# Kernel tuning notes

Hardware: AMD Instinct MI355X
Metric: run time of the kernel (lower is better)

Reference implementation:

```python
import jax, jax.numpy as jnp
import numpy as np

IMAGE_SIZE = 800
OUT = 50          # feature map size
FEAT = 512
SCALES = (2.0, 4.0, 6.0)
RATIOS = (0.5, 1.0, 1.5)
A = len(SCALES) * len(RATIOS)          # 9 anchors per cell
POS_THR, NEG_THR = 0.7, 0.3
W_CONF, W_REG = 1.0, 5.0
SCALE = IMAGE_SIZE // OUT              # 16, stride of feature map


def _anchor_base():
    # order: ratio outer loop, scale inner loop (matches get_anchor_base)
    ws = jnp.array([s * r for r in RATIOS for s in SCALES], jnp.float32)  # [A]
    hs = jnp.array([s for r in RATIOS for s in SCALES], jnp.float32)      # [A]
    cx = (jnp.arange(OUT, dtype=jnp.float32) + 0.5)[:, None, None]        # grid dim0 -> x
    cy = (jnp.arange(OUT, dtype=jnp.float32) + 0.5)[None, :, None]        # grid dim1 -> y
    xmin = jnp.clip(cx - ws / 2, 0.0, OUT)
    xmax = jnp.clip(cx + ws / 2, 0.0, OUT)
    ymin = jnp.clip(cy - hs / 2, 0.0, OUT)
    ymax = jnp.clip(cy + hs / 2, 0.0, OUT)
    shp = (OUT, OUT, A)
    base = jnp.stack([jnp.broadcast_to(xmin, shp), jnp.broadcast_to(ymin, shp),
                      jnp.broadcast_to(xmax, shp), jnp.broadcast_to(ymax, shp)], axis=-1)
    return base.reshape(-1, 4)         # [N,4], N = OUT*OUT*A = 22500


def _iou(anchors, gt):
    # anchors [N,4], gt [B,M,4] (xyxy) -> iou [B,N,M]
    a = anchors[None, :, None, :]
    g = gt[:, None, :, :]
    ix1 = jnp.maximum(a[..., 0], g[..., 0]); iy1 = jnp.maximum(a[..., 1], g[..., 1])
    ix2 = jnp.minimum(a[..., 2], g[..., 2]); iy2 = jnp.minimum(a[..., 3], g[..., 3])
    inter = jnp.clip(ix2 - ix1, 0.0) * jnp.clip(iy2 - iy1, 0.0)
    area_a = (a[..., 2] - a[..., 0]) * (a[..., 3] - a[..., 1])
    area_g = (g[..., 2] - g[..., 0]) * (g[..., 3] - g[..., 1])
    return inter / (area_a + area_g - inter + 1e-8)


def _smooth_l1(d):
    ad = jnp.abs(d)
    return jnp.where(ad < 1.0, 0.5 * d * d, ad - 0.5)


def setup_inputs() -> dict:
    key = jax.random.key(0)
    ks = jax.random.split(key, 8)
    B, M = 16, 16
    features = jax.random.normal(ks[0], (B, FEAT, OUT, OUT), jnp.float32)
    # valid GT boxes in image coords: centers in [100,700], sizes in [32,200]
    cxy = jax.random.uniform(ks[1], (B, M, 2), jnp.float32, 100.0, 700.0)
    wh = jax.random.uniform(ks[2], (B, M, 2), jnp.float32, 32.0, 200.0)
    x1y1 = jnp.clip(cxy - wh / 2, 0.0, IMAGE_SIZE)
    x2y2 = jnp.clip(cxy + wh / 2, 0.0, IMAGE_SIZE)
    gt_boxes = jnp.concatenate([x1y1, x2y2], axis=-1)
    w1 = jax.random.normal(ks[3], (FEAT, FEAT, 3, 3), jnp.float32) * 0.02
    b1 = jnp.zeros((FEAT,), jnp.float32)
    w_cls = jax.random.normal(ks[4], (A, FEAT), jnp.float32) * 0.02
    b_cls = jnp.zeros((A,), jnp.float32)
    w_box = jax.random.normal(ks[5], (4 * A, FEAT), jnp.float32) * 0.02
    b_box = jnp.zeros((4 * A,), jnp.float32)
    return {"features": features, "gt_boxes": gt_boxes, "w1": w1, "b1": b1,
            "w_cls": w_cls, "b_cls": b_cls, "w_box": w_box, "b_box": b_box}


def reference(features, gt_boxes, w1, b1, w_cls, b_cls, w_box, b_box):
    B = features.shape[0]
    anchors = _anchor_base()                                   # [N,4]
    N = anchors.shape[0]

    # --- conv tower ---
    x = jax.lax.conv_general_dilated(features, w1, (1, 1), 'SAME') + b1[None, :, None, None]
    cls_map = jnp.einsum('bchw,ac->bahw', x, w_cls) + b_cls[None, :, None, None]   # [B,A,H,W]
    box_map = jnp.einsum('bchw,dc->bdhw', x, w_box) + b_box[None, :, None, None]   # [B,4A,H,W]
    logits = jnp.transpose(cls_map, (0, 2, 3, 1)).reshape(B, N)                    # [B,N]
    pred_off = jnp.transpose(box_map.reshape(B, A, 4, OUT, OUT), (0, 3, 4, 1, 2)).reshape(B, N, 4)

    # --- project gt to feature-map (anchor) coords, 'p2a' ---
    gt = gt_boxes / SCALE                                       # [B,M,4]

    # --- anchor/GT assignment ---
    iou = _iou(anchors, gt)                                     # [B,N,M]
    max_per_gt = jnp.max(iou, axis=1, keepdims=True)            # best anchor per gt
    pos_mask = ((iou == max_per_gt) & (max_per_gt > 0)) | (iou > POS_THR)  # [B,N,M]
    pos_mask = pos_mask.astype(jnp.float32)
    n_pos = jnp.maximum(pos_mask.sum(), 1.0)

    # --- gt offsets (standard tx,ty,tw,th) for every (anchor,gt) pair ---
    acx = (anchors[:, 0] + anchors[:, 2]) / 2
    acy = (anchors[:, 1] + anchors[:, 3]) / 2
    aw = jnp.maximum(anchors[:, 2] - anchors[:, 0], 1e-6)
    ah = jnp.maximum(anchors[:, 3] - anchors[:, 1], 1e-6)
    gcx = (gt[..., 0] + gt[..., 2]) / 2                         # [B,M]
    gcy = (gt[..., 1] + gt[..., 3]) / 2
    gw = jnp.maximum(gt[..., 2] - gt[..., 0], 1e-6)
    gh = jnp.maximum(gt[..., 3] - gt[..., 1], 1e-6)
    tx = (gcx[:, None, :] - acx[None, :, None]) / aw[None, :, None]   # [B,N,M]
    ty = (gcy[:, None, :] - acy[None, :, None]) / ah[None, :, None]
    tw = jnp.log(gw[:, None, :] / aw[None, :, None])
    th = jnp.log(gh[:, None, :] / ah[None, :, None])
    gt_off = jnp.stack([tx, ty, tw, th], axis=-1)               # [B,N,M,4]

    diff = gt_off - pred_off[:, :, None, :]
    reg_loss = (pos_mask[..., None] * _smooth_l1(diff)).sum() / (4.0 * n_pos)

    # --- classification loss: BCE-with-logits; positives=1, negatives=0 ---
    pos_loss = (pos_mask * jax.nn.softplus(-logits)[:, :, None]).sum() / n_pos
    neg_anchor = jnp.all(iou < NEG_THR, axis=2).astype(jnp.float32)   # [B,N]
    n_neg = jnp.maximum(neg_anchor.sum(), 1.0)
    neg_loss = (neg_anchor * jax.nn.softplus(logits)).sum() / n_neg
    cls_loss = 0.5 * (pos_loss + neg_loss)

    total_rpn_loss = W_CONF * cls_loss + W_REG * reg_loss

    # --- proposals from predicted offsets for all anchors ---
    pcx = acx[None, :] + pred_off[..., 0] * aw[None, :]
    pcy = acy[None, :] + pred_off[..., 1] * ah[None, :]
    pw = aw[None, :] * jnp.exp(pred_off[..., 2])
    ph = ah[None, :] * jnp.exp(pred_off[..., 3])
    proposals = jnp.stack([pcx - pw / 2, pcy - ph / 2, pcx + pw / 2, pcy + ph / 2], axis=-1)  # [B,N,4]

    return total_rpn_loss, proposals
```

## Files before the change

kernel.cpp:

```cpp
#include <hip/hip_runtime.h>
#include <hip/hip_bf16.h>
#include <stdint.h>


using bf16x8 = __attribute__((ext_vector_type(8))) __bf16;
using f32x4  = __attribute__((ext_vector_type(4))) float;

#define FT_CHUNK_STRIDE 2768896
#define W2_CHUNK_B 27648

__device__ __forceinline__ unsigned short f2bf(float f) {
  union { float f; unsigned u; } x; x.f = f;
  unsigned r = x.u + 0x7fffu + ((x.u >> 16) & 1u);
  return (unsigned short)(r >> 16);
}

__device__ __forceinline__ void gl_lds16(const void* g, void* l) {
  __builtin_amdgcn_global_load_lds(
      (const __attribute__((address_space(1))) void*)g,
      (__attribute__((address_space(3))) void*)l, 16, 0, 0);
}

__device__ __forceinline__ float sl1(float d) {
  float ad = fabsf(d);
  return ad < 1.f ? 0.5f * d * d : ad - 0.5f;
}
__device__ __forceinline__ float softplus_f(float x) {
  return fmaxf(x, 0.f) + log1pf(expf(-fabsf(x)));
}

__device__ __forceinline__ void anchor_strict(int n, float& ax1, float& ay1,
                                              float& ax2, float& ay2) {
  int ii = n / 450;
  int rem = n - ii * 450;
  int jj = rem / 9;
  int a  = rem - jj * 9;
  const float SC[3] = {2.f, 4.f, 6.f};
  const float RA[3] = {0.5f, 1.f, 1.5f};
  float w = __fmul_rn(SC[a % 3], RA[a / 3]);
  float h = SC[a % 3];
  float cx = __fadd_rn((float)ii, 0.5f);
  float cy = __fadd_rn((float)jj, 0.5f);
  float wh = __fmul_rn(w, 0.5f), hh = __fmul_rn(h, 0.5f);
  ax1 = fminf(fmaxf(__fsub_rn(cx, wh), 0.f), 50.f);
  ax2 = fminf(fmaxf(__fadd_rn(cx, wh), 0.f), 50.f);
  ay1 = fminf(fmaxf(__fsub_rn(cy, hh), 0.f), 50.f);
  ay2 = fminf(fmaxf(__fadd_rn(cy, hh), 0.f), 50.f);
}
__device__ __forceinline__ float iou_pre(float ax1, float ay1, float ax2, float ay2,
                                         float aarea, const float* __restrict__ s) {
  float ix1 = fmaxf(ax1, s[0]), iy1 = fmaxf(ay1, s[1]);
  float ix2 = fminf(ax2, s[2]), iy2 = fminf(ay2, s[3]);
  float inter = __fmul_rn(fmaxf(__fsub_rn(ix2, ix1), 0.f),
                          fmaxf(__fsub_rn(iy2, iy1), 0.f));
  float denom = __fadd_rn(__fsub_rn(__fadd_rn(aarea, s[4]), inter), 1e-8f);
  return __fdiv_rn(inter, denom);
}

__global__ __launch_bounds__(256, 6) void k1a(const float* __restrict__ feat,
                                              char* __restrict__ featT2) {
  __shared__ __align__(16) unsigned short sT[64 * 132];
  const int bx = blockIdx.x;
  const int tid = threadIdx.x;
  const int tile = bx % 41;
  const int rest = bx / 41;
  const int g    = rest & 3;
  const int b    = rest >> 2;
  if (tile == 40) {
    uint4 z = {0, 0, 0, 0};
    for (int u = tid; u < 204 * 4; u += 256) {
      int p = u & 255; if (p >= 204) p -= 204;
      int c4 = u / 204;
      int ip, jp;
      if (p < 52)       { ip = 0;       jp = p; }
      else if (p < 104) { ip = 51;      jp = p - 52; }
      else if (p < 154) { ip = p - 103; jp = 0; }
      else              { ip = p - 153; jp = 51; }
      char* dst = featT2 + (size_t)(g * 4 + c4) * FT_CHUNK_STRIDE
                + (size_t)(b * 2704 + ip * 52 + jp) * 64;
      *(uint4*)(dst)      = z;
      *(uint4*)(dst + 16) = z;
      *(uint4*)(dst + 32) = z;
      *(uint4*)(dst + 48) = z;
    }
    return;
  }
  const int pos0 = tile * 64;
  const float* fb = feat + (size_t)b * 1280000 + (size_t)(g * 128) * 2500;
  const int pq = tid & 15;
  const int cq = tid >> 4;
  const int p  = pos0 + pq * 4;
  float vv[2][4][4];
  if (p + 3 < 2500) {
#pragma unroll
    for (int it = 0; it < 2; ++it)
#pragma unroll
      for (int q = 0; q < 4; ++q) {
        float4 v = *(const float4*)(fb + (size_t)(it * 64 + cq * 4 + q) * 2500 + p);
        vv[it][q][0] = v.x; vv[it][q][1] = v.y;
        vv[it][q][2] = v.z; vv[it][q][3] = v.w;
      }
  } else {
#pragma unroll
    for (int it = 0; it < 2; ++it)
#pragma unroll
      for (int q = 0; q < 4; ++q)
#pragma unroll
        for (int e = 0; e < 4; ++e)
          vv[it][q][e] = fb[(size_t)(it * 64 + cq * 4 + q) * 2500 + min(p + e, 2499)];
  }
#pragma unroll
  for (int it = 0; it < 2; ++it) {
#pragma unroll
    for (int pp = 0; pp < 4; ++pp) {
      ushort4 pk;
      pk.x = f2bf(vv[it][0][pp]); pk.y = f2bf(vv[it][1][pp]);
      pk.z = f2bf(vv[it][2][pp]); pk.w = f2bf(vv[it][3][pp]);
      *(ushort4*)&sT[(pq * 4 + pp) * 132 + it * 64 + cq * 4] = pk;
    }
  }
  __syncthreads();
  {
    int ch = tid >> 6, pr = tid & 63;
    int gp = pos0 + pr;
    if (gp < 2500) {
      int i = gp / 50, j = gp - i * 50;
      char* dst = featT2 + (size_t)(g * 4 + ch) * FT_CHUNK_STRIDE
                + (size_t)(b * 2704 + (i + 1) * 52 + (j + 1)) * 64;
      const uint4* src = (const uint4*)&sT[pr * 132 + ch * 32];
      uint4 a0 = src[0], a1 = src[1], a2 = src[2], a3 = src[3];
      *(uint4*)(dst)      = a0;
      *(uint4*)(dst + 16) = a1;
      *(uint4*)(dst + 32) = a2;
      *(uint4*)(dst + 48) = a3;
    }
  }
}

__global__ __launch_bounds__(256, 4) void k1b(const float* __restrict__ w1,
                                              const float* __restrict__ wc,
                                              const float* __restrict__ wb,
                                              const float* __restrict__ b1,
                                              const float* __restrict__ bc,
                                              const float* __restrict__ bbx,
                                              float* __restrict__ part,
                                              float* __restrict__ bias_eff,
                                              const float* __restrict__ gt_boxes,
                                              float* __restrict__ iouBuf,
                                              float* __restrict__ mxPart,
                                              unsigned* __restrict__ accz) {
  __shared__ __align__(16) float sW[48 * 64];
  const int bxr = blockIdx.x;
  const int tid = threadIdx.x;

  if (bxr < 576) {
    if (bxr == 0 && tid < 8) accz[tid] = 0u;
    int cz = bxr / 72, kx = bxr - cz * 72;
#pragma unroll
    for (int q = 0; q < 12; ++q) {
      int idx = tid + q * 256;
      int co = idx >> 6, cl = idx & 63;
      int c = cz * 64 + cl;
      float v = 0.f;
      if (co < 9) v = wc[co * 512 + c];
      else if (co < 45) v = wb[(co - 9) * 512 + c];
      sW[co * 64 + cl] = v;
    }
    __syncthreads();
    const int kmem = kx * 64 + (tid & 63);
    const int coq  = tid >> 6;
    float acc[12];
#pragma unroll
    for (int j = 0; j < 12; ++j) acc[j] = 0.f;
    const float* w1p = w1 + (size_t)(cz * 64) * 4608 + kmem;
    for (int c4 = 0; c4 < 64; c4 += 4) {
      float f0 = w1p[(size_t)(c4 + 0) * 4608];
      float f1 = w1p[(size_t)(c4 + 1) * 4608];
      float f2 = w1p[(size_t)(c4 + 2) * 4608];
      float f3 = w1p[(size_t)(c4 + 3) * 4608];
#pragma unroll
      for (int j = 0; j < 12; ++j) {
        float4 wv = *(const float4*)&sW[(coq * 12 + j) * 64 + c4];
        acc[j] += wv.x * f0 + wv.y * f1 + wv.z * f2 + wv.w * f3;
      }
    }
    float* dst = part + (size_t)cz * 221184 + kmem;
#pragma unroll
    for (int j = 0; j < 12; ++j) dst[(size_t)(coq * 12 + j) * 4608] = acc[j];
    return;
  }

  if (bxr < 624) {
    int co = bxr - 576;
    int l = tid;
    if (l >= 64) return;
    float s = 0.f;
#pragma unroll
    for (int q = 0; q < 8; ++q) {
      int c = q * 64 + l;
      float wv = co < 9 ? wc[co * 512 + c] : (co < 45 ? wb[(co - 9) * 512 + c] : 0.f);
      s += wv * b1[c];
    }
    for (int o = 32; o; o >>= 1) s += __shfl_down(s, o, 64);
    if (l == 0)
      bias_eff[co] = s + (co < 9 ? bc[co] : (co < 45 ? bbx[co - 9] : 0.f));
    return;
  }

  {
    int q = bxr - 624;
    int b = q / 88, nb = q - b * 88;
    int n = nb * 256 + tid;
    float (*sgg)[5] = (float(*)[5])sW;
    float (*red)[16] = (float(*)[16])(sW + 128);
    if (tid < 16) {
      const float* g = gt_boxes + (b * 16 + tid) * 4;
      float gx1 = __fmul_rn(g[0], 0.0625f), gy1 = __fmul_rn(g[1], 0.0625f);
      float gx2 = __fmul_rn(g[2], 0.0625f), gy2 = __fmul_rn(g[3], 0.0625f);
      sgg[tid][0] = gx1; sgg[tid][1] = gy1; sgg[tid][2] = gx2; sgg[tid][3] = gy2;
      sgg[tid][4] = __fmul_rn(__fsub_rn(gx2, gx1), __fsub_rn(gy2, gy1));
    }
    __syncthreads();
    float lm[16];
#pragma unroll
    for (int m = 0; m < 16; ++m) lm[m] = 0.f;
    if (n < 22500) {
      float ax1, ay1, ax2, ay2;
      anchor_strict(n, ax1, ay1, ax2, ay2);
      float aarea = __fmul_rn(__fsub_rn(ax2, ax1), __fsub_rn(ay2, ay1));
#pragma unroll
      for (int m = 0; m < 16; ++m)
        lm[m] = iou_pre(ax1, ay1, ax2, ay2, aarea, sgg[m]);
      float* dv = iouBuf + (size_t)(b * 22500 + n) * 16;
#pragma unroll
      for (int v4 = 0; v4 < 4; ++v4) {
        float4 pk;
        pk.x = lm[v4 * 4 + 0]; pk.y = lm[v4 * 4 + 1];
        pk.z = lm[v4 * 4 + 2]; pk.w = lm[v4 * 4 + 3];
        *(float4*)(dv + v4 * 4) = pk;
      }
    }
#pragma unroll
    for (int m = 0; m < 16; ++m) {
      float v = lm[m];
      for (int o = 32; o; o >>= 1) v = fmaxf(v, __shfl_down(v, o, 64));
      if ((tid & 63) == 0) red[tid >> 6][m] = v;
    }
    __syncthreads();
    if (tid < 16) {
      float v = fmaxf(fmaxf(red[0][tid], red[1][tid]),
                      fmaxf(red[2][tid], red[3][tid]));
      mxPart[(b * 16 + tid) * 88 + nb] = v;
    }
  }
}

__global__ __launch_bounds__(256) void k2(const float* __restrict__ part,
                                          unsigned short* __restrict__ w2,
                                          const float* __restrict__ mxPart,
                                          unsigned* __restrict__ mx) {
  if (blockIdx.x == 864) {
    int t = threadIdx.x;
    const float* mp = mxPart + t * 88;
    float v = 0.f;
    for (int k = 0; k < 88; ++k) v = fmaxf(v, mp[k]);
    mx[t] = __float_as_uint(v);
    return;
  }
  int co = blockIdx.x / 18, kx = blockIdx.x - co * 18;
  int kmem = kx * 256 + threadIdx.x;
  const float* p = part + (size_t)co * 4608 + kmem;
  float s = 0.f;
#pragma unroll
  for (int cz = 0; cz < 8; ++cz) s += p[(size_t)cz * 221184];
  int ci = kmem / 9, tap = kmem - ci * 9;
  int c = ci >> 5, e = ci & 31;
  int boff = c * W2_CHUNK_B + tap * 3072 + (co >> 4) * 1024 + (co & 15) * 64
           + ((((e >> 3) ^ co) & 3) << 4) + ((e & 7) << 1);
  w2[boff >> 1] = f2bf(s);
}

__global__ __launch_bounds__(256, 2) void k3(const char* __restrict__ featT2,
                                             const char* __restrict__ w2g,
                                             const float* __restrict__ beff,
                                             float* __restrict__ oh) {
  __shared__ __align__(16) char sF[2][11264];
  __shared__ __align__(16) char sA[2][27648];
  const int tid = threadIdx.x, lane = tid & 63, w = tid >> 6;
  const int bx0 = blockIdx.x;
  const int bx = ((bx0 & 7) << 6) | (bx0 >> 3);
  const int b = bx >> 5, tl = bx & 31, tr = tl >> 3, tc = tl & 7;
  const int i0 = tr * 13 - (tr == 3 ? 1 : 0);
  const int TI = (tr >= 2) ? 12 : 13;
  const int TJ = (tc < 2) ? 7 : 6;
  const int j0 = (tc < 2) ? tc * 7 : 14 + (tc - 2) * 6;
  const int TJ2 = TJ + 2;
  const int mcount = TI * TJ;
  const int pieces = (TI + 2) * TJ2 * 5;

  const char* srcF[3];
#pragma unroll
  for (int k = 0; k < 3; ++k) {
    int s = w * 3 + k;
    int pi = s * 64 + lane;
    if (pi >= pieces) pi = pieces - 1;
    int pos = pi / 5, pc = pi - pos * 5;
    if (pc > 3) pc = 3;
    int hi = pos / TJ2, hj = pos - hi * TJ2;
    srcF[k] = featT2 + (size_t)(b * 2704 + (i0 + hi) * 52 + (j0 + hj)) * 64 + pc * 16;
  }
  int idxB[2];
#pragma unroll
  for (int bf = 0; bf < 2; ++bf) {
    int p = (w * 2 + bf) * 16 + (lane & 15);
    if (p >= mcount) p = mcount - 1;
    int di = p / TJ, dj = p - di * TJ;
    idxB[bf] = (di * TJ2 + dj) * 80 + (lane >> 4) * 16;
  }
  const int aoff = (lane & 15) * 64 + ((((lane >> 4) ^ lane) & 3) << 4);
  int toff[9];
#pragma unroll
  for (int tp = 0; tp < 9; ++tp) toff[tp] = ((tp / 3) * TJ2 + (tp % 3)) * 80;

  f32x4 acc[3][2] = {};

  auto stage = [&](int c, int pb) {
    size_t coff = (size_t)c * FT_CHUNK_STRIDE;
#pragma unroll
    for (int k = 0; k < 3; ++k) {
      int s = w * 3 + k;
      if (s < 11) gl_lds16(srcF[k] + coff, sF[pb] + s * 1024);
    }
#pragma unroll
    for (int k = 0; k < 7; ++k) {
      int s = w + 4 * k;
      if (s < 27)
        gl_lds16(w2g + (size_t)c * W2_CHUNK_B + s * 1024 + lane * 16, sA[pb] + s * 1024);
    }
  };

  stage(0, 0);
  __builtin_amdgcn_s_waitcnt(0);
  __syncthreads();

  for (int c = 0; c < 16; ++c) {
    int pb = c & 1;
    if (c < 15) stage(c + 1, pb ^ 1);
    const char* fA = sA[pb];
    const char* fB = sF[pb];
#pragma unroll
    for (int tp = 0; tp < 9; ++tp) {
      bf16x8 av[3], bv[2];
#pragma unroll
      for (int cf = 0; cf < 3; ++cf)
        av[cf] = *(const bf16x8*)(fA + tp * 3072 + cf * 1024 + aoff);
#pragma unroll
      for (int bf = 0; bf < 2; ++bf)
        bv[bf] = *(const bf16x8*)(fB + idxB[bf] + toff[tp]);
#pragma unroll
      for (int cf = 0; cf < 3; ++cf)
#pragma unroll
        for (int bf = 0; bf < 2; ++bf)
          acc[cf][bf] = __builtin_amdgcn_mfma_f32_16x16x32_bf16(av[cf], bv[bf], acc[cf][bf], 0, 0, 0);
    }
    __builtin_amdgcn_s_waitcnt(0);
    __syncthreads();
  }

  f32x4 bias[3];
#pragma unroll
  for (int cf = 0; cf < 3; ++cf)
    bias[cf] = *(const f32x4*)(beff + cf * 16 + (lane >> 4) * 4);
#pragma unroll
  for (int bf = 0; bf < 2; ++bf) {
    int p = (w * 2 + bf) * 16 + (lane & 15);
    if (p >= mcount) continue;
    int di = p / TJ, dj = p - di * TJ;
    int gm = (b * 50 + i0 + di) * 50 + (j0 + dj);
#pragma unroll
    for (int cf = 0; cf < 3; ++cf) {
      f32x4 v = acc[cf][bf];
#pragma unroll
      for (int r = 0; r < 4; ++r) v[r] += bias[cf][r];
      *(f32x4*)(oh + (size_t)gm * 48 + cf * 16 + (lane >> 4) * 4) = v;
    }
  }
}

__global__ __launch_bounds__(256, 2) void k4(const float* __restrict__ gt_boxes,
                                             const unsigned* __restrict__ mxbuf,
                                             const float* __restrict__ iouBuf,
                                             const float* __restrict__ oh,
                                             float* __restrict__ accum,
                                             float* __restrict__ dout) {
  const int tid = threadIdx.x;
  const int b = blockIdx.y;
  __shared__ float sg[16][5];
  if (tid < 16) {
    const float* g = gt_boxes + (b * 16 + tid) * 4;
    float gx1 = __fmul_rn(g[0], 0.0625f), gy1 = __fmul_rn(g[1], 0.0625f);
    float gx2 = __fmul_rn(g[2], 0.0625f), gy2 = __fmul_rn(g[3], 0.0625f);
    sg[tid][0] = (gx1 + gx2) * 0.5f;
    sg[tid][1] = (gy1 + gy2) * 0.5f;
    sg[tid][2] = fmaxf(gx2 - gx1, 1e-6f);
    sg[tid][3] = fmaxf(gy2 - gy1, 1e-6f);
    sg[tid][4] = __uint_as_float(mxbuf[b * 16 + tid]);
  }
  __syncthreads();

  const int n = blockIdx.x * 256 + tid;
  float s_np = 0.f, s_reg = 0.f, s_pos = 0.f, s_nc = 0.f, s_nl = 0.f;
  if (n < 22500) {
    float ax1, ay1, ax2, ay2;
    anchor_strict(n, ax1, ay1, ax2, ay2);
    float acx = (ax1 + ax2) * 0.5f, acy = (ay1 + ay2) * 0.5f;
    float aw = fmaxf(ax2 - ax1, 1e-6f), ah = fmaxf(ay2 - ay1, 1e-6f);
    int ii = n / 450, rem = n - ii * 450, jj = rem / 9, a = rem - jj * 9;
    const float* row = oh + ((size_t)(b * 2500 + ii * 50 + jj)) * 48;
    float logit = row[a];
    float p0 = row[9 + a * 4], p1 = row[10 + a * 4];
    float p2 = row[11 + a * 4], p3 = row[12 + a * 4];
    const float* iv = iouBuf + (size_t)(b * 22500 + n) * 16;
    float io[16];
#pragma unroll
    for (int v4 = 0; v4 < 4; ++v4) {
      float4 v = *(const float4*)(iv + v4 * 4);
      io[v4 * 4 + 0] = v.x; io[v4 * 4 + 1] = v.y;
      io[v4 * 4 + 2] = v.z; io[v4 * 4 + 3] = v.w;
    }
    int npos = 0;
    bool allneg = true;
#pragma unroll
    for (int m = 0; m < 16; ++m) {
      float iou = io[m];
      float mxv = sg[m][4];
      bool pos = ((iou == mxv) && (mxv > 0.f)) || (iou > 0.7f);
      if (iou >= 0.3f) allneg = false;
      if (pos) {
        ++npos;
        float tx = (sg[m][0] - acx) / aw, ty = (sg[m][1] - acy) / ah;
        float twv = logf(sg[m][2] / aw), thv = logf(sg[m][3] / ah);
        s_reg += sl1(tx - p0) + sl1(ty - p1) + sl1(twv - p2) + sl1(thv - p3);
      }
    }
    s_np = (float)npos;
    s_pos = (float)npos * softplus_f(-logit);
    if (allneg) { s_nc = 1.f; s_nl = softplus_f(logit); }
    float pcx = acx + p0 * aw, pcy = acy + p1 * ah;
    float pw = aw * expf(p2), ph = ah * expf(p3);
    float* o = dout + 1 + ((size_t)b * 22500 + n) * 4;
    o[0] = pcx - pw * 0.5f;
    o[1] = pcy - ph * 0.5f;
    o[2] = pcx + pw * 0.5f;
    o[3] = pcy + ph * 0.5f;
  }
  float vals[5] = {s_np, s_reg, s_pos, s_nc, s_nl};
  __shared__ float red[4][5];
#pragma unroll
  for (int q = 0; q < 5; ++q) {
    float v = vals[q];
    for (int o = 32; o; o >>= 1) v += __shfl_down(v, o, 64);
    if ((tid & 63) == 0) red[tid >> 6][q] = v;
  }
  __syncthreads();
  if (tid < 5) {
    float v = red[0][tid] + red[1][tid] + red[2][tid] + red[3][tid];
    atomicAdd(accum + tid, v);
  }
  __syncthreads();
  if (tid == 0) {
    __threadfence();
    unsigned old = atomicAdd((unsigned*)(accum + 5), 1u);
    if (old == 1407u) {
      float np = fmaxf(atomicAdd(accum + 0, 0.f), 1.f);
      float rg = atomicAdd(accum + 1, 0.f);
      float pp = atomicAdd(accum + 2, 0.f);
      float nn = fmaxf(atomicAdd(accum + 3, 0.f), 1.f);
      float nl = atomicAdd(accum + 4, 0.f);
      dout[0] = 0.5f * (pp / np + nl / nn) + 5.f * (rg / (4.f * np));
    }
  }
}

extern "C" void kernel_launch(void* const* d_in, const int* in_sizes, int n_in,
                              void* d_out, int out_size, void* d_ws, size_t ws_size,
                              hipStream_t stream) {
  const float* features = (const float*)d_in[0];
  const float* gt_boxes = (const float*)d_in[1];
  const float* w1    = (const float*)d_in[2];
  const float* b1    = (const float*)d_in[3];
  const float* w_cls = (const float*)d_in[4];
  const float* b_cls = (const float*)d_in[5];
  const float* w_box = (const float*)d_in[6];
  const float* b_box = (const float*)d_in[7];
  float* out = (float*)d_out;
  char* ws = (char*)d_ws;

  char*           featT2 = ws;
  unsigned short* w2     = (unsigned short*)(ws + 44302336);
  float*          wpart  = (float*)(ws + 44855296);
  float*          oh     = (float*)(ws + 51933184);
  float*          beff   = (float*)(ws + 59613184);
  float*          mxPart = (float*)(ws + 59613376);
  unsigned*       mx     = (unsigned*)(ws + 59703488);
  float*          accum  = (float*)(ws + 59704512);
  float*          iouBuf = (float*)(ws + 59704576);

  k1b<<<2032, 256, 0, stream>>>(w1, w_cls, w_box, b1, b_cls, b_box, wpart, beff,
                                gt_boxes, iouBuf, mxPart, (unsigned*)accum);
  k2<<<865, 256, 0, stream>>>(wpart, w2, mxPart, mx);
  k1a<<<2624, 256, 0, stream>>>(features, featT2);
  k3<<<512, 256, 0, stream>>>(featT2, (const char*)w2, beff, oh);
  k4<<<dim3(88, 16), 256, 0, stream>>>(gt_boxes, mx, iouBuf, oh, accum, out);
}
```

Baseline: 291.2 us.

## Merge preprocessing kernels into one launch and fold weight reduction inline

Combines the feature transpose, weight-folding, bias and IoU kernels into a single heterogeneous kernel with coarsened blocks (four work units per block). The weight fold now reduces all 512 channels per block and writes swizzled bf16 weights directly, which removes the partial-sum buffer and the separate reduction kernel. The per-GT max reduction moves into the loss kernel, which also processes four chunks per block with fewer atomics. This cuts launches and intermediate traffic, but the weight-fold path now runs on only 72 blocks with long serial loops, so it may become a critical-path straggler.

```diff
diff --git a/kernel.cpp b/kernel.cpp
--- a/kernel.cpp
+++ b/kernel.cpp
@@ -57,162 +57,185 @@
   return __fdiv_rn(inter, denom);
 }
 
-__global__ __launch_bounds__(256, 6) void k1a(const float* __restrict__ feat,
-                                              char* __restrict__ featT2) {
-  __shared__ __align__(16) unsigned short sT[64 * 132];
-  const int bx = blockIdx.x;
-  const int tid = threadIdx.x;
-  const int tile = bx % 41;
-  const int rest = bx / 41;
-  const int g    = rest & 3;
-  const int b    = rest >> 2;
-  if (tile == 40) {
-    uint4 z = {0, 0, 0, 0};
-    for (int u = tid; u < 204 * 4; u += 256) {
-      int p = u & 255; if (p >= 204) p -= 204;
-      int c4 = u / 204;
-      int ip, jp;
-      if (p < 52)       { ip = 0;       jp = p; }
-      else if (p < 104) { ip = 51;      jp = p - 52; }
-      else if (p < 154) { ip = p - 103; jp = 0; }
-      else              { ip = p - 153; jp = 51; }
-      char* dst = featT2 + (size_t)(g * 4 + c4) * FT_CHUNK_STRIDE
-                + (size_t)(b * 2704 + ip * 52 + jp) * 64;
-      *(uint4*)(dst)      = z;
-      *(uint4*)(dst + 16) = z;
-      *(uint4*)(dst + 32) = z;
-      *(uint4*)(dst + 48) = z;
-    }
-    return;
-  }
-  const int pos0 = tile * 64;
-  const float* fb = feat + (size_t)b * 1280000 + (size_t)(g * 128) * 2500;
-  const int pq = tid & 15;
-  const int cq = tid >> 4;
-  const int p  = pos0 + pq * 4;
-  float vv[2][4][4];
-  if (p + 3 < 2500) {
-#pragma unroll
-    for (int it = 0; it < 2; ++it)
-#pragma unroll
-      for (int q = 0; q < 4; ++q) {
-        float4 v = *(const float4*)(fb + (size_t)(it * 64 + cq * 4 + q) * 2500 + p);
-        vv[it][q][0] = v.x; vv[it][q][1] = v.y;
-        vv[it][q][2] = v.z; vv[it][q][3] = v.w;
-      }
-  } else {
-#pragma unroll
-    for (int it = 0; it < 2; ++it)
-#pragma unroll
-      for (int q = 0; q < 4; ++q)
-#pragma unroll
-        for (int e = 0; e < 4; ++e)
-          vv[it][q][e] = fb[(size_t)(it * 64 + cq * 4 + q) * 2500 + min(p + e, 2499)];
-  }
-#pragma unroll
-  for (int it = 0; it < 2; ++it) {
-#pragma unroll
-    for (int pp = 0; pp < 4; ++pp) {
-      ushort4 pk;
-      pk.x = f2bf(vv[it][0][pp]); pk.y = f2bf(vv[it][1][pp]);
-      pk.z = f2bf(vv[it][2][pp]); pk.w = f2bf(vv[it][3][pp]);
-      *(ushort4*)&sT[(pq * 4 + pp) * 132 + it * 64 + cq * 4] = pk;
-    }
-  }
-  __syncthreads();
-  {
-    int ch = tid >> 6, pr = tid & 63;
-    int gp = pos0 + pr;
-    if (gp < 2500) {
-      int i = gp / 50, j = gp - i * 50;
-      char* dst = featT2 + (size_t)(g * 4 + ch) * FT_CHUNK_STRIDE
-                + (size_t)(b * 2704 + (i + 1) * 52 + (j + 1)) * 64;
-      const uint4* src = (const uint4*)&sT[pr * 132 + ch * 32];
-      uint4 a0 = src[0], a1 = src[1], a2 = src[2], a3 = src[3];
-      *(uint4*)(dst)      = a0;
-      *(uint4*)(dst + 16) = a1;
-      *(uint4*)(dst + 32) = a2;
-      *(uint4*)(dst + 48) = a3;
-    }
-  }
-}
-
-__global__ __launch_bounds__(256, 4) void k1b(const float* __restrict__ w1,
-                                              const float* __restrict__ wc,
-                                              const float* __restrict__ wb,
-                                              const float* __restrict__ b1,
-                                              const float* __restrict__ bc,
-                                              const float* __restrict__ bbx,
-                                              float* __restrict__ part,
-                                              float* __restrict__ bias_eff,
-                                              const float* __restrict__ gt_boxes,
-                                              float* __restrict__ iouBuf,
-                                              float* __restrict__ mxPart,
-                                              unsigned* __restrict__ accz) {
-  __shared__ __align__(16) float sW[48 * 64];
+__global__ __launch_bounds__(256, 4) void kA(const float* __restrict__ feat,
+                                             char* __restrict__ featT2,
+                                             const float* __restrict__ w1,
+                                             const float* __restrict__ wc,
+                                             const float* __restrict__ wb,
+                                             const float* __restrict__ b1,
+                                             const float* __restrict__ bc,
+                                             const float* __restrict__ bbx,
+                                             unsigned short* __restrict__ w2,
+                                             float* __restrict__ bias_eff,
+                                             const float* __restrict__ gt_boxes,
+                                             float* __restrict__ iouBuf,
+                                             float* __restrict__ mxPart,
+                                             unsigned* __restrict__ accz) {
+  __shared__ __align__(16) char smem[24576];
   const int bxr = blockIdx.x;
   const int tid = threadIdx.x;
 
-  if (bxr < 576) {
-    if (bxr == 0 && tid < 8) accz[tid] = 0u;
-    int cz = bxr / 72, kx = bxr - cz * 72;
-#pragma unroll
-    for (int q = 0; q < 12; ++q) {
+  if (bxr < 656) {
+    unsigned short* sT = (unsigned short*)smem;
+#pragma unroll 1
+    for (int ku = 0; ku < 4; ++ku) {
+      if (ku) __syncthreads();
+      const int u = bxr * 4 + ku;
+      const int tile = u % 41;
+      const int rest = u / 41;
+      const int g    = rest & 3;
+      const int b    = rest >> 2;
+      if (tile == 40) {
+        uint4 z = {0, 0, 0, 0};
+        for (int uu = tid; uu < 204 * 4; uu += 256) {
+          int p = uu & 255; if (p >= 204) p -= 204;
+          int c4 = uu / 204;
+          int ip, jp;
+          if (p < 52)       { ip = 0;       jp = p; }
+          else if (p < 104) { ip = 51;      jp = p - 52; }
+          else if (p < 154) { ip = p - 103; jp = 0; }
+          else              { ip = p - 153; jp = 51; }
+          char* dst = featT2 + (size_t)(g * 4 + c4) * FT_CHUNK_STRIDE
+                    + (size_t)(b * 2704 + ip * 52 + jp) * 64;
+          *(uint4*)(dst)      = z;
+          *(uint4*)(dst + 16) = z;
+          *(uint4*)(dst + 32) = z;
+          *(uint4*)(dst + 48) = z;
+        }
+        continue;
+      }
+      const int pos0 = tile * 64;
+      const float* fb = feat + (size_t)b * 1280000 + (size_t)(g * 128) * 2500;
+      const int pq = tid & 15;
+      const int cq = tid >> 4;
+      const int p  = pos0 + pq * 4;
+      float vv[2][4][4];
+      if (p + 3 < 2500) {
+#pragma unroll
+        for (int it = 0; it < 2; ++it)
+#pragma unroll
+          for (int q = 0; q < 4; ++q) {
+            float4 v = *(const float4*)(fb + (size_t)(it * 64 + cq * 4 + q) * 2500 + p);
+            vv[it][q][0] = v.x; vv[it][q][1] = v.y;
+            vv[it][q][2] = v.z; vv[it][q][3] = v.w;
+          }
+      } else {
+#pragma unroll
+        for (int it = 0; it < 2; ++it)
+#pragma unroll
+          for (int q = 0; q < 4; ++q)
+#pragma unroll
+            for (int e = 0; e < 4; ++e)
+              vv[it][q][e] = fb[(size_t)(it * 64 + cq * 4 + q) * 2500 + min(p + e, 2499)];
+      }
+#pragma unroll
+      for (int it = 0; it < 2; ++it) {
+#pragma unroll
+        for (int pp = 0; pp < 4; ++pp) {
+          ushort4 pk;
+          pk.x = f2bf(vv[it][0][pp]); pk.y = f2bf(vv[it][1][pp]);
+          pk.z = f2bf(vv[it][2][pp]); pk.w = f2bf(vv[it][3][pp]);
+          *(ushort4*)&sT[(pq * 4 + pp) * 132 + it * 64 + cq * 4] = pk;
+        }
+      }
+      __syncthreads();
+      {
+        int ch = tid >> 6, pr = tid & 63;
+        int gp = pos0 + pr;
+        if (gp < 2500) {
+          int i = gp / 50, j = gp - i * 50;
+          char* dst = featT2 + (size_t)(g * 4 + ch) * FT_CHUNK_STRIDE
+                    + (size_t)(b * 2704 + (i + 1) * 52 + (j + 1)) * 64;
+          const uint4* src = (const uint4*)&sT[pr * 132 + ch * 32];
+          uint4 a0 = src[0], a1 = src[1], a2 = src[2], a3 = src[3];
+          *(uint4*)(dst)      = a0;
+          *(uint4*)(dst + 16) = a1;
+          *(uint4*)(dst + 32) = a2;
+          *(uint4*)(dst + 48) = a3;
+        }
+      }
+    }
+    return;
+  }
+
+  if (bxr < 728) {
+    if (bxr == 656 && tid < 8) accz[tid] = 0u;
+    int bx2 = bxr - 656;
+    int kx = bx2 % 18, coq = bx2 / 18;
+    float* swq = (float*)smem;
+#pragma unroll
+    for (int q = 0; q < 24; ++q) {
       int idx = tid + q * 256;
-      int co = idx >> 6, cl = idx & 63;
-      int c = cz * 64 + cl;
+      int j = idx >> 9, c = idx & 511;
+      int co = coq * 12 + j;
       float v = 0.f;
       if (co < 9) v = wc[co * 512 + c];
       else if (co < 45) v = wb[(co - 9) * 512 + c];
-      sW[co * 64 + cl] = v;
+      swq[j * 512 + c] = v;
     }
     __syncthreads();
-    const int kmem = kx * 64 + (tid & 63);
-    const int coq  = tid >> 6;
-    float acc[12];
-#pragma unroll
-    for (int j = 0; j < 12; ++j) acc[j] = 0.f;
-    const float* w1p = w1 + (size_t)(cz * 64) * 4608 + kmem;
-    for (int c4 = 0; c4 < 64; c4 += 4) {
-      float f0 = w1p[(size_t)(c4 + 0) * 4608];
-      float f1 = w1p[(size_t)(c4 + 1) * 4608];
-      float f2 = w1p[(size_t)(c4 + 2) * 4608];
-      float f3 = w1p[(size_t)(c4 + 3) * 4608];
-#pragma unroll
-      for (int j = 0; j < 12; ++j) {
-        float4 wv = *(const float4*)&sW[(coq * 12 + j) * 64 + c4];
-        acc[j] += wv.x * f0 + wv.y * f1 + wv.z * f2 + wv.w * f3;
-      }
-    }
-    float* dst = part + (size_t)cz * 221184 + kmem;
-#pragma unroll
-    for (int j = 0; j < 12; ++j) dst[(size_t)(coq * 12 + j) * 4608] = acc[j];
+    const int kmem = kx * 256 + tid;
+    float s[12];
+#pragma unroll
+    for (int j = 0; j < 12; ++j) s[j] = 0.f;
+    const float* w1p = w1 + kmem;
+    for (int cz = 0; cz < 8; ++cz) {
+      float acc[12];
+#pragma unroll
+      for (int j = 0; j < 12; ++j) acc[j] = 0.f;
+      for (int c4 = 0; c4 < 64; c4 += 4) {
+        int cb = cz * 64 + c4;
+        float f0 = w1p[(size_t)(cb + 0) * 4608];
+        float f1 = w1p[(size_t)(cb + 1) * 4608];
+        float f2 = w1p[(size_t)(cb + 2) * 4608];
+        float f3 = w1p[(size_t)(cb + 3) * 4608];
+#pragma unroll
+        for (int j = 0; j < 12; ++j) {
+          float4 wv = *(const float4*)&swq[j * 512 + cb];
+          acc[j] += wv.x * f0 + wv.y * f1 + wv.z * f2 + wv.w * f3;
+        }
+      }
+#pragma unroll
+      for (int j = 0; j < 12; ++j) s[j] += acc[j];
+    }
+    int ci = kmem / 9, tap = kmem - ci * 9;
+    int c = ci >> 5, e = ci & 31;
+#pragma unroll
+    for (int j = 0; j < 12; ++j) {
+      int co = coq * 12 + j;
+      int boff = c * W2_CHUNK_B + tap * 3072 + (co >> 4) * 1024 + (co & 15) * 64
+               + ((((e >> 3) ^ co) & 3) << 4) + ((e & 7) << 1);
+      w2[boff >> 1] = f2bf(s[j]);
+    }
     return;
   }
 
-  if (bxr < 624) {
-    int co = bxr - 576;
+  if (bxr < 744) {
     int l = tid;
     if (l >= 64) return;
-    float s = 0.f;
-#pragma unroll
-    for (int q = 0; q < 8; ++q) {
-      int c = q * 64 + l;
-      float wv = co < 9 ? wc[co * 512 + c] : (co < 45 ? wb[(co - 9) * 512 + c] : 0.f);
-      s += wv * b1[c];
-    }
-    for (int o = 32; o; o >>= 1) s += __shfl_down(s, o, 64);
-    if (l == 0)
-      bias_eff[co] = s + (co < 9 ? bc[co] : (co < 45 ? bbx[co - 9] : 0.f));
+#pragma unroll 1
+    for (int j = 0; j < 3; ++j) {
+      int co = (bxr - 728) * 3 + j;
+      float s = 0.f;
+#pragma unroll
+      for (int q = 0; q < 8; ++q) {
+        int c = q * 64 + l;
+        float wv = co < 9 ? wc[co * 512 + c] : (co < 45 ? wb[(co - 9) * 512 + c] : 0.f);
+        s += wv * b1[c];
+      }
+      for (int o = 32; o; o >>= 1) s += __shfl_down(s, o, 64);
+      if (l == 0)
+        bias_eff[co] = s + (co < 9 ? bc[co] : (co < 45 ? bbx[co - 9] : 0.f));
+    }
     return;
   }
 
   {
-    int q = bxr - 624;
-    int b = q / 88, nb = q - b * 88;
-    int n = nb * 256 + tid;
-    float (*sgg)[5] = (float(*)[5])sW;
-    float (*red)[16] = (float(*)[16])(sW + 128);
+    int bx3 = bxr - 744;
+    int q0 = bx3 * 4;
+    int b = q0 / 88;
+    float (*sgg)[5] = (float(*)[5])smem;
+    float (*red)[16] = (float(*)[16])((float*)smem + 128);
     if (tid < 16) {
       const float* g = gt_boxes + (b * 16 + tid) * 4;
       float gx1 = __fmul_rn(g[0], 0.0625f), gy1 = __fmul_rn(g[1], 0.0625f);
@@ -221,66 +244,48 @@
       sgg[tid][4] = __fmul_rn(__fsub_rn(gx2, gx1), __fsub_rn(gy2, gy1));
     }
     __syncthreads();
-    float lm[16];
-#pragma unroll
-    for (int m = 0; m < 16; ++m) lm[m] = 0.f;
-    if (n < 22500) {
-      float ax1, ay1, ax2, ay2;
-      anchor_strict(n, ax1, ay1, ax2, ay2);
-      float aarea = __fmul_rn(__fsub_rn(ax2, ax1), __fsub_rn(ay2, ay1));
-#pragma unroll
-      for (int m = 0; m < 16; ++m)
-        lm[m] = iou_pre(ax1, ay1, ax2, ay2, aarea, sgg[m]);
-      float* dv = iouBuf + (size_t)(b * 22500 + n) * 16;
-#pragma unroll
-      for (int v4 = 0; v4 < 4; ++v4) {
-        float4 pk;
-        pk.x = lm[v4 * 4 + 0]; pk.y = lm[v4 * 4 + 1];
-        pk.z = lm[v4 * 4 + 2]; pk.w = lm[v4 * 4 + 3];
-        *(float4*)(dv + v4 * 4) = pk;
-      }
-    }
-#pragma unroll
-    for (int m = 0; m < 16; ++m) {
-      float v = lm[m];
-      for (int o = 32; o; o >>= 1) v = fmaxf(v, __shfl_down(v, o, 64));
-      if ((tid & 63) == 0) red[tid >> 6][m] = v;
-    }
-    __syncthreads();
-    if (tid < 16) {
-      float v = fmaxf(fmaxf(red[0][tid], red[1][tid]),
-                      fmaxf(red[2][tid], red[3][tid]));
-      mxPart[(b * 16 + tid) * 88 + nb] = v;
-    }
-  }
-}
-
-__global__ __launch_bounds__(256) void k2(const float* __restrict__ part,
-                                          unsigned short* __restrict__ w2,
-                                          const float* __restrict__ mxPart,
-                                          unsigned* __restrict__ mx) {
-  if (blockIdx.x == 864) {
-    int t = threadIdx.x;
-    const float* mp = mxPart + t * 88;
-    float v = 0.f;
-    for (int k = 0; k < 88; ++k) v = fmaxf(v, mp[k]);
-    mx[t] = __float_as_uint(v);
-    return;
-  }
-  int co = blockIdx.x / 18, kx = blockIdx.x - co * 18;
-  int kmem = kx * 256 + threadIdx.x;
-  const float* p = part + (size_t)co * 4608 + kmem;
-  float s = 0.f;
-#pragma unroll
-  for (int cz = 0; cz < 8; ++cz) s += p[(size_t)cz * 221184];
-  int ci = kmem / 9, tap = kmem - ci * 9;
-  int c = ci >> 5, e = ci & 31;
-  int boff = c * W2_CHUNK_B + tap * 3072 + (co >> 4) * 1024 + (co & 15) * 64
-           + ((((e >> 3) ^ co) & 3) << 4) + ((e & 7) << 1);
-  w2[boff >> 1] = f2bf(s);
-}
-
-__global__ __launch_bounds__(256, 2) void k3(const char* __restrict__ featT2,
+#pragma unroll 1
+    for (int ku = 0; ku < 4; ++ku) {
+      int q = q0 + ku;
+      int nb = q - b * 88;
+      int n = nb * 256 + tid;
+      float lm[16];
+#pragma unroll
+      for (int m = 0; m < 16; ++m) lm[m] = 0.f;
+      if (n < 22500) {
+        float ax1, ay1, ax2, ay2;
+        anchor_strict(n, ax1, ay1, ax2, ay2);
+        float aarea = __fmul_rn(__fsub_rn(ax2, ax1), __fsub_rn(ay2, ay1));
+#pragma unroll
+        for (int m = 0; m < 16; ++m)
+          lm[m] = iou_pre(ax1, ay1, ax2, ay2, aarea, sgg[m]);
+        float* dv = iouBuf + (size_t)(b * 22500 + n) * 16;
+#pragma unroll
+        for (int v4 = 0; v4 < 4; ++v4) {
+          float4 pk;
+          pk.x = lm[v4 * 4 + 0]; pk.y = lm[v4 * 4 + 1];
+          pk.z = lm[v4 * 4 + 2]; pk.w = lm[v4 * 4 + 3];
+          *(float4*)(dv + v4 * 4) = pk;
+        }
+      }
+#pragma unroll
+      for (int m = 0; m < 16; ++m) {
+        float v = lm[m];
+        for (int o = 32; o; o >>= 1) v = fmaxf(v, __shfl_down(v, o, 64));
+        if ((tid & 63) == 0) red[tid >> 6][m] = v;
+      }
+      __syncthreads();
+      if (tid < 16) {
+        float v = fmaxf(fmaxf(red[0][tid], red[1][tid]),
+                        fmaxf(red[2][tid], red[3][tid]));
+        mxPart[(b * 16 + tid) * 88 + nb] = v;
+      }
+      __syncthreads();
+    }
+  }
+}
+
+__global__ __launch_bounds__(256, 2) void kB(const char* __restrict__ featT2,
                                              const char* __restrict__ w2g,
                                              const float* __restrict__ beff,
                                              float* __restrict__ oh) {
@@ -387,15 +392,24 @@
   }
 }
 
-__global__ __launch_bounds__(256, 2) void k4(const float* __restrict__ gt_boxes,
-                                             const unsigned* __restrict__ mxbuf,
+__global__ __launch_bounds__(256, 4) void kC(const float* __restrict__ gt_boxes,
+                                             const float* __restrict__ mxPart,
                                              const float* __restrict__ iouBuf,
                                              const float* __restrict__ oh,
                                              float* __restrict__ accum,
                                              float* __restrict__ dout) {
   const int tid = threadIdx.x;
   const int b = blockIdx.y;
+  const int bx = blockIdx.x;
   __shared__ float sg[16][5];
+  __shared__ float redmx[16][16];
+  {
+    int m = tid & 15, part = tid >> 4;
+    float v = 0.f;
+    for (int nb = part; nb < 88; nb += 16)
+      v = fmaxf(v, mxPart[(b * 16 + m) * 88 + nb]);
+    redmx[part][m] = v;
+  }
   if (tid < 16) {
     const float* g = gt_boxes + (b * 16 + tid) * 4;
     float gx1 = __fmul_rn(g[0], 0.0625f), gy1 = __fmul_rn(g[1], 0.0625f);
@@ -404,13 +418,21 @@
     sg[tid][1] = (gy1 + gy2) * 0.5f;
     sg[tid][2] = fmaxf(gx2 - gx1, 1e-6f);
     sg[tid][3] = fmaxf(gy2 - gy1, 1e-6f);
-    sg[tid][4] = __uint_as_float(mxbuf[b * 16 + tid]);
   }
   __syncthreads();
-
-  const int n = blockIdx.x * 256 + tid;
+  if (tid < 16) {
+    float v = redmx[0][tid];
+#pragma unroll
+    for (int p = 1; p < 16; ++p) v = fmaxf(v, redmx[p][tid]);
+    sg[tid][4] = v;
+  }
+  __syncthreads();
+
   float s_np = 0.f, s_reg = 0.f, s_pos = 0.f, s_nc = 0.f, s_nl = 0.f;
-  if (n < 22500) {
+#pragma unroll 1
+  for (int cch = 0; cch < 4; ++cch) {
+    const int n = (bx * 4 + cch) * 256 + tid;
+    if (n >= 22500) continue;
     float ax1, ay1, ax2, ay2;
     anchor_strict(n, ax1, ay1, ax2, ay2);
     float acx = (ax1 + ax2) * 0.5f, acy = (ay1 + ay2) * 0.5f;
@@ -443,9 +465,9 @@
         s_reg += sl1(tx - p0) + sl1(ty - p1) + sl1(twv - p2) + sl1(thv - p3);
       }
     }
-    s_np = (float)npos;
-    s_pos = (float)npos * softplus_f(-logit);
-    if (allneg) { s_nc = 1.f; s_nl = softplus_f(logit); }
+    s_np += (float)npos;
+    s_pos += (float)npos * softplus_f(-logit);
+    if (allneg) { s_nc += 1.f; s_nl += softplus_f(logit); }
     float pcx = acx + p0 * aw, pcy = acy + p1 * ah;
     float pw = aw * expf(p2), ph = ah * expf(p3);
     float* o = dout + 1 + ((size_t)b * 22500 + n) * 4;
@@ -454,6 +476,7 @@
     o[2] = pcx + pw * 0.5f;
     o[3] = pcy + ph * 0.5f;
   }
+
   float vals[5] = {s_np, s_reg, s_pos, s_nc, s_nl};
   __shared__ float red[4][5];
 #pragma unroll
@@ -471,7 +494,7 @@
   if (tid == 0) {
     __threadfence();
     unsigned old = atomicAdd((unsigned*)(accum + 5), 1u);
-    if (old == 1407u) {
+    if (old == 351u) {
       float np = fmaxf(atomicAdd(accum + 0, 0.f), 1.f);
       float rg = atomicAdd(accum + 1, 0.f);
       float pp = atomicAdd(accum + 2, 0.f);
@@ -498,18 +521,15 @@
 
   char*           featT2 = ws;
   unsigned short* w2     = (unsigned short*)(ws + 44302336);
-  float*          wpart  = (float*)(ws + 44855296);
-  float*          oh     = (float*)(ws + 51933184);
-  float*          beff   = (float*)(ws + 59613184);
-  float*          mxPart = (float*)(ws + 59613376);
-  unsigned*       mx     = (unsigned*)(ws + 59703488);
-  float*          accum  = (float*)(ws + 59704512);
-  float*          iouBuf = (float*)(ws + 59704576);
-
-  k1b<<<2032, 256, 0, stream>>>(w1, w_cls, w_box, b1, b_cls, b_box, wpart, beff,
-                                gt_boxes, iouBuf, mxPart, (unsigned*)accum);
-  k2<<<865, 256, 0, stream>>>(wpart, w2, mxPart, mx);
-  k1a<<<2624, 256, 0, stream>>>(features, featT2);
-  k3<<<512, 256, 0, stream>>>(featT2, (const char*)w2, beff, oh);
-  k4<<<dim3(88, 16), 256, 0, stream>>>(gt_boxes, mx, iouBuf, oh, accum, out);
-}
+  float*          oh     = (float*)(ws + 44855296);
+  float*          beff   = (float*)(ws + 52535296);
+  float*          mxPart = (float*)(ws + 52535488);
+  float*          accum  = (float*)(ws + 52625600);
+  float*          iouBuf = (float*)(ws + 52625664);
+
+  kA<<<1096, 256, 0, stream>>>(features, featT2, w1, w_cls, w_box, b1, b_cls,
+                               b_box, w2, beff, gt_boxes, iouBuf, mxPart,
+                               (unsigned*)accum);
+  kB<<<512, 256, 0, stream>>>(featT2, (const char*)w2, beff, oh);
+  kC<<<dim3(22, 16), 256, 0, stream>>>(gt_boxes, mxPart, iouBuf, oh, accum, out);
+}
```

Result: no change. 292.7 us (+0.5%).
